# Optimization experiments

Hardware: AMD Instinct MI355X
Metric: run time of the kernel (lower is better)

## Reference

```python
import jax, jax.numpy as jnp
import numpy as np

B, N = 64, 196
D1, D2, H = 512, 2048, 512


def setup_inputs() -> dict:
    key = jax.random.key(0)
    ks = jax.random.split(key, 8)
    s1 = 1.0 / np.sqrt(D1)
    s2 = 1.0 / np.sqrt(D2)
    sh = 1.0 / np.sqrt(H)
    return {
        "input1": jax.random.normal(ks[0], (B, D1), jnp.float32),
        "input2": jax.random.normal(ks[1], (B, N, D2), jnp.float32),
        "W1": jax.random.uniform(ks[2], (D1, H), jnp.float32, -s1, s1),
        "b1": jax.random.uniform(ks[3], (H,), jnp.float32, -s1, s1),
        "W2": jax.random.uniform(ks[4], (D2, H), jnp.float32, -s2, s2),
        "b2": jax.random.uniform(ks[5], (H,), jnp.float32, -s2, s2),
        "Wf": jax.random.uniform(ks[6], (H, 1), jnp.float32, -sh, sh),
        "bf": jax.random.uniform(ks[7], (1,), jnp.float32, -sh, sh),
    }


def reference(input1, input2, W1, b1, W2, b2, Wf, bf):
    # enc1: [B, H]; enc2: [B, N, H]
    enc1 = input1 @ W1 + b1
    enc2 = jnp.einsum("bnd,dh->bnh", input2, W2) + b2
    # additive (Bahdanau) score: relu(enc2 + enc1[:,None]) @ Wf -> [B, N]
    scores = (jax.nn.relu(enc2 + enc1[:, None, :]) @ Wf)[..., 0] + bf[0]
    alpha = jax.nn.softmax(scores, axis=1)  # softmax over N regions
    att = jnp.einsum("bnd,bn->bd", input2, alpha)  # weighted sum of raw features
    return att, alpha
```

## Files before the change

### kernel.cpp

```cpp
#include <hip/hip_runtime.h>
#include <hip/hip_bf16.h>
#include <stdint.h>

#define BB 64
#define NN 196
#define D1c 512
#define D2c 2048
#define HHc 512
#define MM (BB*NN)

typedef __attribute__((ext_vector_type(8))) short bf16x8;
typedef __attribute__((ext_vector_type(4))) float f32x4;

__device__ inline ushort f2bf(float f){
  uint32_t u = __float_as_uint(f);
  u += 0x7fff + ((u >> 16) & 1);
  return (ushort)(u >> 16);
}
__device__ inline uint32_t pack2(float a, float b){
  return (uint32_t)f2bf(a) | ((uint32_t)f2bf(b) << 16);
}

__global__ __launch_bounds__(256) void w2t_kernel(const float* __restrict__ W2,
                                                  ushort* __restrict__ w2t){
  __shared__ float tile[64][65];
  const int kt = blockIdx.x;
  const int ht = blockIdx.y;
  const int t = threadIdx.x;
  const int tr = t >> 4;
  const int tc = (t & 15) * 4;
  #pragma unroll
  for (int p = 0; p < 4; ++p){
    int k = p*16 + tr;
    float4 v = *(const float4*)(W2 + (size_t)(kt*64 + k)*HHc + ht*64 + tc);
    tile[k][tc] = v.x; tile[k][tc+1] = v.y; tile[k][tc+2] = v.z; tile[k][tc+3] = v.w;
  }
  __syncthreads();
  #pragma unroll
  for (int p = 0; p < 4; ++p){
    int h = p*16 + tr;
    ushort4 o;
    o.x = f2bf(tile[tc  ][h]);
    o.y = f2bf(tile[tc+1][h]);
    o.z = f2bf(tile[tc+2][h]);
    o.w = f2bf(tile[tc+3][h]);
    *(ushort4*)(w2t + (size_t)(ht*64 + h)*D2c + kt*64 + tc) = o;
  }
}

__global__ __launch_bounds__(128) void enc1_kernel(const float* __restrict__ in1,
                                                   const float* __restrict__ W1,
                                                   const float* __restrict__ b1,
                                                   float* __restrict__ enc1){
  __shared__ float s1[D1c];
  const int b = blockIdx.x;
  const int ht = blockIdx.y;
  const int t = threadIdx.x;
  ((float4*)s1)[t] = ((const float4*)(in1 + (size_t)b*D1c))[t];
  __syncthreads();
  const int h = ht*128 + t;
  float acc = b1[h];
  #pragma unroll 8
  for (int d = 0; d < D1c; ++d)
    acc += s1[d] * W1[(size_t)d*HHc + h];
  enc1[b*HHc + h] = acc;
}

__global__ __launch_bounds__(256,2) void score_gemm(
    const float*  __restrict__ in2,
    const ushort* __restrict__ w2t,
    const float*  __restrict__ b2,
    const float*  __restrict__ wf,
    const float*  __restrict__ enc1,
    float*        __restrict__ scores)
{
  __shared__ ushort As[2][64*64];
  __shared__ ushort Bs[2][256*64];

  const int t = threadIdx.x;
  const int p  = blockIdx.x;
  const int lg = (p & 7) * 49 + (p >> 3);
  const int h0 = (lg & 1) * 256;
  const int m0 = (lg >> 1) * 64;

  const int wave = t >> 6, lane = t & 63;
  const int l15 = lane & 15, l4 = lane >> 4;

  const int arow = t >> 2;
  const int aq   = t & 3;
  const float* aBase = in2 + (size_t)(m0 + arow)*D2c + aq*16;
  const int ac0 = ((aq*2    ) ^ (arow & 7)) << 3;
  const int ac1 = ((aq*2 + 1) ^ (arow & 7)) << 3;

  const int bl_r = lane >> 3;
  const int bl_c = (lane & 7) ^ bl_r;

  float b2v[4], wfv[4];
  #pragma unroll
  for (int hf = 0; hf < 4; ++hf){
    int hc = h0 + wave*64 + hf*16 + l15;
    b2v[hf] = b2[hc]; wfv[hf] = wf[hc];
  }

  f32x4 acc[4][4];
  #pragma unroll
  for (int i = 0; i < 4; ++i)
    #pragma unroll
    for (int j = 0; j < 4; ++j) acc[i][j] = (f32x4)0.f;

  float4 aReg[4];

#define A_LOAD(kt)                                                           \
  { _Pragma("unroll")                                                        \
    for (int j = 0; j < 4; ++j)                                              \
      aReg[j] = *(const float4*)(aBase + (kt)*64 + j*4); }

#define A_WRITE(buf)                                                         \
  { uint4 w0, w1;                                                            \
    w0.x = pack2(aReg[0].x, aReg[0].y); w0.y = pack2(aReg[0].z, aReg[0].w);  \
    w0.z = pack2(aReg[1].x, aReg[1].y); w0.w = pack2(aReg[1].z, aReg[1].w);  \
    w1.x = pack2(aReg[2].x, aReg[2].y); w1.y = pack2(aReg[2].z, aReg[2].w);  \
    w1.z = pack2(aReg[3].x, aReg[3].y); w1.w = pack2(aReg[3].z, aReg[3].w);  \
    *(uint4*)(As[buf] + arow*64 + ac0) = w0;                                 \
    *(uint4*)(As[buf] + arow*64 + ac1) = w1; }

#define B_GLDS(kt, buf)                                                      \
  { _Pragma("unroll")                                                        \
    for (int i = 0; i < 8; ++i){                                             \
      const ushort* src = w2t + (size_t)(h0 + wave*64 + i*8 + bl_r)*D2c      \
                          + (kt)*64 + bl_c*8;                                \
      __builtin_amdgcn_global_load_lds(                                      \
          (const __attribute__((address_space(1))) uint32_t*)src,            \
          (__attribute__((address_space(3))) uint32_t*)(Bs[buf] + (wave*64 + i*8)*64), \
          16, 0, 0); } }

#define COMPUTE(buf)                                                         \
  { _Pragma("unroll")                                                        \
    for (int kk = 0; kk < 2; ++kk){                                          \
      bf16x8 af[4], bfr[4];                                                  \
      _Pragma("unroll")                                                      \
      for (int mf = 0; mf < 4; ++mf){                                        \
        int r = mf*16 + l15, c = kk*4 + l4;                                  \
        af[mf] = *(const bf16x8*)(As[buf] + r*64 + ((c ^ (r & 7)) << 3)); }  \
      _Pragma("unroll")                                                      \
      for (int hf = 0; hf < 4; ++hf){                                        \
        int r = wave*64 + hf*16 + l15, c = kk*4 + l4;                        \
        bfr[hf] = *(const bf16x8*)(Bs[buf] + r*64 + ((c ^ (r & 7)) << 3)); } \
      _Pragma("unroll")                                                      \
      for (int mf = 0; mf < 4; ++mf)                                         \
        _Pragma("unroll")                                                    \
        for (int hf = 0; hf < 4; ++hf)                                       \
          acc[mf][hf] = __builtin_amdgcn_mfma_f32_16x16x32_bf16(             \
              af[mf], bfr[hf], acc[mf][hf], 0, 0, 0); } }

#define SB0() __builtin_amdgcn_sched_barrier(0)
#define BAR() { SB0(); __builtin_amdgcn_s_barrier(); SB0(); }

  A_LOAD(0);
  SB0();
  B_GLDS(0, 0);
  asm volatile("s_waitcnt vmcnt(8)" ::: "memory");
  SB0();
  A_WRITE(0);
  asm volatile("s_waitcnt lgkmcnt(0)" ::: "memory");
  BAR();

  for (int kt = 0; kt < 31; ++kt){
    const int cur = kt & 1;
    A_LOAD(kt + 1);
    SB0();
    B_GLDS(kt + 1, cur ^ 1);
    asm volatile("s_waitcnt vmcnt(12)" ::: "memory");
    BAR();
    COMPUTE(cur);
    asm volatile("s_waitcnt vmcnt(8)" ::: "memory");
    SB0();
    A_WRITE(cur ^ 1);
    asm volatile("s_waitcnt lgkmcnt(0)" ::: "memory");
    BAR();
  }
  asm volatile("s_waitcnt vmcnt(0)" ::: "memory");
  BAR();
  COMPUTE(1);

  #pragma unroll
  for (int mf = 0; mf < 4; ++mf){
    #pragma unroll
    for (int r = 0; r < 4; ++r){
      int m = m0 + mf*16 + l4*4 + r;
      int b = m / NN;
      const float* e1 = enc1 + (size_t)b*HHc + h0 + wave*64 + l15;
      float s = 0.f;
      #pragma unroll
      for (int hf = 0; hf < 4; ++hf){
        float v = acc[mf][hf][r] + b2v[hf] + e1[hf*16];
        s += fmaxf(v, 0.f) * wfv[hf];
      }
      s += __shfl_xor(s, 1); s += __shfl_xor(s, 2);
      s += __shfl_xor(s, 4); s += __shfl_xor(s, 8);
      if (l15 == 0) atomicAdd(&scores[m], s);
    }
  }
#undef A_LOAD
#undef A_WRITE
#undef B_GLDS
#undef COMPUTE
#undef SB0
#undef BAR
}

__global__ __launch_bounds__(64) void softmax_kernel(const float* __restrict__ scores,
                                                     float* __restrict__ alpha){
  const int b = blockIdx.x, t = threadIdx.x;
  const float* s = scores + b*NN;
  float x[4]; float mx = -1e30f;
  #pragma unroll
  for (int i = 0; i < 4; ++i){
    int n = t + i*64;
    x[i] = (n < NN) ? s[n] : -1e30f;
    mx = fmaxf(mx, x[i]);
  }
  #pragma unroll
  for (int o = 1; o < 64; o <<= 1) mx = fmaxf(mx, __shfl_xor(mx, o));
  float sum = 0.f;
  #pragma unroll
  for (int i = 0; i < 4; ++i){
    int n = t + i*64;
    float e = (n < NN) ? __expf(x[i] - mx) : 0.f;
    x[i] = e; sum += e;
  }
  #pragma unroll
  for (int o = 1; o < 64; o <<= 1) sum += __shfl_xor(sum, o);
  float inv = 1.f / sum;
  #pragma unroll
  for (int i = 0; i < 4; ++i){
    int n = t + i*64;
    if (n < NN) alpha[b*NN + n] = x[i] * inv;
  }
}

__global__ __launch_bounds__(256) void att_kernel(const float* __restrict__ in2,
                                                  const float* __restrict__ alpha,
                                                  float* __restrict__ att){
  __shared__ float sal[NN];
  const int b = blockIdx.y;
  const int t = threadIdx.x;
  if (t < NN) sal[t] = alpha[b*NN + t];
  __syncthreads();
  const int d = blockIdx.x*256 + t;
  const float* src = in2 + (size_t)b*NN*D2c + d;
  float acc = 0.f;
  #pragma unroll 7
  for (int n = 0; n < NN; ++n)
    acc += src[(size_t)n*D2c] * sal[n];
  att[(size_t)b*D2c + d] = acc;
}

extern "C" void kernel_launch(void* const* d_in, const int* in_sizes, int n_in,
                              void* d_out, int out_size, void* d_ws, size_t ws_size,
                              hipStream_t stream){
  (void)in_sizes; (void)n_in; (void)out_size; (void)ws_size;
  const float* input1 = (const float*)d_in[0];
  const float* input2 = (const float*)d_in[1];
  const float* W1     = (const float*)d_in[2];
  const float* b1     = (const float*)d_in[3];
  const float* W2     = (const float*)d_in[4];
  const float* b2     = (const float*)d_in[5];
  const float* Wf     = (const float*)d_in[6];

  float* out   = (float*)d_out;
  float* att   = out;
  float* alpha = out + BB*D2c;

  char*   ws     = (char*)d_ws;
  ushort* w2t    = (ushort*)ws;
  float*  enc1   = (float*)(ws + 2*1024*1024);
  float*  scores = (float*)(ws + 2*1024*1024 + 131072);

  hipMemsetAsync(scores, 0, MM*sizeof(float), stream);
  w2t_kernel<<<dim3(32, 8), 256, 0, stream>>>(W2, w2t);
  enc1_kernel<<<dim3(BB, 4), 128, 0, stream>>>(input1, W1, b1, enc1);
  score_gemm<<<dim3(392), 256, 0, stream>>>(input2, w2t, b2, Wf, enc1, scores);
  softmax_kernel<<<dim3(BB), 64, 0, stream>>>(scores, alpha);
  att_kernel<<<dim3(8, BB), 256, 0, stream>>>(input2, alpha, att);
}
```

Measured before the change: 112.8 us.

## Pre-swizzle W2 into MFMA fragment layout and load B directly to registers

```diff
diff --git a/kernel.cpp b/kernel.cpp
--- a/kernel.cpp
+++ b/kernel.cpp
@@ -24,27 +24,30 @@
 __global__ __launch_bounds__(256) void w2t_kernel(const float* __restrict__ W2,
                                                   ushort* __restrict__ w2t){
   __shared__ float tile[64][65];
-  const int kt = blockIdx.x;
-  const int ht = blockIdx.y;
+  const int ktb = blockIdx.x;
+  const int ht  = blockIdx.y;
   const int t = threadIdx.x;
   const int tr = t >> 4;
   const int tc = (t & 15) * 4;
   #pragma unroll
   for (int p = 0; p < 4; ++p){
     int k = p*16 + tr;
-    float4 v = *(const float4*)(W2 + (size_t)(kt*64 + k)*HHc + ht*64 + tc);
+    float4 v = *(const float4*)(W2 + (size_t)(ktb*64 + k)*HHc + ht*64 + tc);
     tile[k][tc] = v.x; tile[k][tc+1] = v.y; tile[k][tc+2] = v.z; tile[k][tc+3] = v.w;
   }
   __syncthreads();
   #pragma unroll
-  for (int p = 0; p < 4; ++p){
-    int h = p*16 + tr;
+  for (int pp = 0; pp < 4; ++pp){
+    int hl = pp*16 + tr;
     ushort4 o;
-    o.x = f2bf(tile[tc  ][h]);
-    o.y = f2bf(tile[tc+1][h]);
-    o.z = f2bf(tile[tc+2][h]);
-    o.w = f2bf(tile[tc+3][h]);
-    *(ushort4*)(w2t + (size_t)(ht*64 + h)*D2c + kt*64 + tc) = o;
+    o.x = f2bf(tile[tc  ][hl]);
+    o.y = f2bf(tile[tc+1][hl]);
+    o.z = f2bf(tile[tc+2][hl]);
+    o.w = f2bf(tile[tc+3][hl]);
+    size_t addr = (size_t)(ht*4 + pp)*32768 + (size_t)ktb*1024
+                + (size_t)((tc>>5)&1)*512 + (size_t)((tc>>3)&3)*128
+                + (size_t)tr*8 + (tc & 4);
+    *(ushort4*)(w2t + addr) = o;
   }
 }
 
@@ -66,7 +69,7 @@
   enc1[b*HHc + h] = acc;
 }
 
-__global__ __launch_bounds__(256,2) void score_gemm(
+__global__ __launch_bounds__(256) void score_gemm(
     const float*  __restrict__ in2,
     const ushort* __restrict__ w2t,
     const float*  __restrict__ b2,
@@ -75,7 +78,6 @@
     float*        __restrict__ scores)
 {
   __shared__ ushort As[2][64*64];
-  __shared__ ushort Bs[2][256*64];
 
   const int t = threadIdx.x;
   const int p  = blockIdx.x;
@@ -92,8 +94,7 @@
   const int ac0 = ((aq*2    ) ^ (arow & 7)) << 3;
   const int ac1 = ((aq*2 + 1) ^ (arow & 7)) << 3;
 
-  const int bl_r = lane >> 3;
-  const int bl_c = (lane & 7) ^ bl_r;
+  const ushort* bBase = w2t + (size_t)h0*2048 + (size_t)wave*131072 + lane*8;
 
   float b2v[4], wfv[4];
   #pragma unroll
@@ -109,11 +110,17 @@
     for (int j = 0; j < 4; ++j) acc[i][j] = (f32x4)0.f;
 
   float4 aReg[4];
+  bf16x8 bA[8], bB[8];
 
 #define A_LOAD(kt)                                                           \
   { _Pragma("unroll")                                                        \
     for (int j = 0; j < 4; ++j)                                              \
       aReg[j] = *(const float4*)(aBase + (kt)*64 + j*4); }
+
+#define B_LOAD(kt, B)                                                        \
+  { _Pragma("unroll")                                                        \
+    for (int f = 0; f < 8; ++f)                                              \
+      B[f] = *(const bf16x8*)(bBase + (f>>1)*32768 + (kt)*1024 + (f&1)*512); }
 
 #define A_WRITE(buf)                                                         \
   { uint4 w0, w1;                                                            \
@@ -124,64 +131,53 @@
     *(uint4*)(As[buf] + arow*64 + ac0) = w0;                                 \
     *(uint4*)(As[buf] + arow*64 + ac1) = w1; }
 
-#define B_GLDS(kt, buf)                                                      \
-  { _Pragma("unroll")                                                        \
-    for (int i = 0; i < 8; ++i){                                             \
-      const ushort* src = w2t + (size_t)(h0 + wave*64 + i*8 + bl_r)*D2c      \
-                          + (kt)*64 + bl_c*8;                                \
-      __builtin_amdgcn_global_load_lds(                                      \
-          (const __attribute__((address_space(1))) uint32_t*)src,            \
-          (__attribute__((address_space(3))) uint32_t*)(Bs[buf] + (wave*64 + i*8)*64), \
-          16, 0, 0); } }
-
-#define COMPUTE(buf)                                                         \
+#define COMPUTE(buf, B)                                                      \
   { _Pragma("unroll")                                                        \
     for (int kk = 0; kk < 2; ++kk){                                          \
-      bf16x8 af[4], bfr[4];                                                  \
+      bf16x8 af[4];                                                          \
       _Pragma("unroll")                                                      \
       for (int mf = 0; mf < 4; ++mf){                                        \
         int r = mf*16 + l15, c = kk*4 + l4;                                  \
         af[mf] = *(const bf16x8*)(As[buf] + r*64 + ((c ^ (r & 7)) << 3)); }  \
       _Pragma("unroll")                                                      \
-      for (int hf = 0; hf < 4; ++hf){                                        \
-        int r = wave*64 + hf*16 + l15, c = kk*4 + l4;                        \
-        bfr[hf] = *(const bf16x8*)(Bs[buf] + r*64 + ((c ^ (r & 7)) << 3)); } \
-      _Pragma("unroll")                                                      \
       for (int mf = 0; mf < 4; ++mf)                                         \
         _Pragma("unroll")                                                    \
         for (int hf = 0; hf < 4; ++hf)                                       \
           acc[mf][hf] = __builtin_amdgcn_mfma_f32_16x16x32_bf16(             \
-              af[mf], bfr[hf], acc[mf][hf], 0, 0, 0); } }
-
-#define SB0() __builtin_amdgcn_sched_barrier(0)
-#define BAR() { SB0(); __builtin_amdgcn_s_barrier(); SB0(); }
+              af[mf], B[hf*2+kk], acc[mf][hf], 0, 0, 0); } }
+
+#define LGKM0() asm volatile("s_waitcnt lgkmcnt(0)" ::: "memory")
+#define SB0()   __builtin_amdgcn_sched_barrier(0)
+#define BAR()   { SB0(); __builtin_amdgcn_s_barrier(); SB0(); }
 
   A_LOAD(0);
-  SB0();
-  B_GLDS(0, 0);
-  asm volatile("s_waitcnt vmcnt(8)" ::: "memory");
-  SB0();
+  B_LOAD(0, bA);
   A_WRITE(0);
-  asm volatile("s_waitcnt lgkmcnt(0)" ::: "memory");
+  LGKM0();
   BAR();
 
-  for (int kt = 0; kt < 31; ++kt){
-    const int cur = kt & 1;
+  #pragma unroll 1
+  for (int kt = 0; kt < 30; kt += 2){
     A_LOAD(kt + 1);
-    SB0();
-    B_GLDS(kt + 1, cur ^ 1);
-    asm volatile("s_waitcnt vmcnt(12)" ::: "memory");
+    B_LOAD(kt + 1, bB);
+    COMPUTE(0, bA);
+    A_WRITE(1);
+    LGKM0();
     BAR();
-    COMPUTE(cur);
-    asm volatile("s_waitcnt vmcnt(8)" ::: "memory");
-    SB0();
-    A_WRITE(cur ^ 1);
-    asm volatile("s_waitcnt lgkmcnt(0)" ::: "memory");
+    A_LOAD(kt + 2);
+    B_LOAD(kt + 2, bA);
+    COMPUTE(1, bB);
+    A_WRITE(0);
+    LGKM0();
     BAR();
   }
-  asm volatile("s_waitcnt vmcnt(0)" ::: "memory");
+  A_LOAD(31);
+  B_LOAD(31, bB);
+  COMPUTE(0, bA);
+  A_WRITE(1);
+  LGKM0();
   BAR();
-  COMPUTE(1);
+  COMPUTE(1, bB);
 
   #pragma unroll
   for (int mf = 0; mf < 4; ++mf){
@@ -202,9 +198,10 @@
     }
   }
 #undef A_LOAD
+#undef B_LOAD
 #undef A_WRITE
-#undef B_GLDS
 #undef COMPUTE
+#undef LGKM0
 #undef SB0
 #undef BAR
 }
```

Result: faster. 105.3 us (-6.7%).

## Enlarge score GEMM tile to 128x256 with 8 waves and hardware bf16 pack

Applied to the files above, without the earlier changes.

```diff
diff --git a/kernel.cpp b/kernel.cpp
--- a/kernel.cpp
+++ b/kernel.cpp
@@ -17,8 +17,10 @@
   u += 0x7fff + ((u >> 16) & 1);
   return (ushort)(u >> 16);
 }
-__device__ inline uint32_t pack2(float a, float b){
-  return (uint32_t)f2bf(a) | ((uint32_t)f2bf(b) << 16);
+__device__ inline uint32_t cvtpk(float lo, float hi){
+  uint32_t r;
+  asm("v_cvt_pk_bf16_f32 %0, %1, %2" : "=v"(r) : "v"(lo), "v"(hi));
+  return r;
 }
 
 __global__ __launch_bounds__(256) void w2t_kernel(const float* __restrict__ W2,
@@ -66,7 +68,7 @@
   enc1[b*HHc + h] = acc;
 }
 
-__global__ __launch_bounds__(256,2) void score_gemm(
+__global__ __launch_bounds__(512,2) void score_gemm(
     const float*  __restrict__ in2,
     const ushort* __restrict__ w2t,
     const float*  __restrict__ b2,
@@ -74,23 +76,24 @@
     const float*  __restrict__ enc1,
     float*        __restrict__ scores)
 {
-  __shared__ ushort As[2][64*64];
+  __shared__ ushort As[2][128*64];
   __shared__ ushort Bs[2][256*64];
 
   const int t = threadIdx.x;
-  const int p  = blockIdx.x;
-  const int lg = (p & 7) * 49 + (p >> 3);
-  const int h0 = (lg & 1) * 256;
-  const int m0 = (lg >> 1) * 64;
+  const int p   = blockIdx.x;
+  const int xcd = p & 7;
+  const int lg  = (xcd < 4 ? xcd*25 : 100 + (xcd-4)*24) + (p >> 3);
+  const int h0  = (lg & 1) * 256;
+  const int m0  = (lg >> 1) * 128;
 
   const int wave = t >> 6, lane = t & 63;
+  const int wm = wave >> 2, whh = wave & 3;
   const int l15 = lane & 15, l4 = lane >> 4;
 
-  const int arow = t >> 2;
-  const int aq   = t & 3;
-  const float* aBase = in2 + (size_t)(m0 + arow)*D2c + aq*16;
-  const int ac0 = ((aq*2    ) ^ (arow & 7)) << 3;
-  const int ac1 = ((aq*2 + 1) ^ (arow & 7)) << 3;
+  const int rA = wave*16 + l4;
+  const float* aBase = in2 + (size_t)(m0 + rA)*D2c + l15*4;
+  const int acw  = l15 >> 1;
+  const int apar = (l15 & 1) * 4;
 
   const int bl_r = lane >> 3;
   const int bl_c = (lane & 7) ^ bl_r;
@@ -98,7 +101,7 @@
   float b2v[4], wfv[4];
   #pragma unroll
   for (int hf = 0; hf < 4; ++hf){
-    int hc = h0 + wave*64 + hf*16 + l15;
+    int hc = h0 + whh*64 + hf*16 + l15;
     b2v[hf] = b2[hc]; wfv[hf] = wf[hc];
   }
 
@@ -113,25 +116,26 @@
 #define A_LOAD(kt)                                                           \
   { _Pragma("unroll")                                                        \
     for (int j = 0; j < 4; ++j)                                              \
-      aReg[j] = *(const float4*)(aBase + (kt)*64 + j*4); }
+      aReg[j] = *(const float4*)(aBase + (size_t)(j*4)*D2c + (kt)*64); }
 
 #define A_WRITE(buf)                                                         \
-  { uint4 w0, w1;                                                            \
-    w0.x = pack2(aReg[0].x, aReg[0].y); w0.y = pack2(aReg[0].z, aReg[0].w);  \
-    w0.z = pack2(aReg[1].x, aReg[1].y); w0.w = pack2(aReg[1].z, aReg[1].w);  \
-    w1.x = pack2(aReg[2].x, aReg[2].y); w1.y = pack2(aReg[2].z, aReg[2].w);  \
-    w1.z = pack2(aReg[3].x, aReg[3].y); w1.w = pack2(aReg[3].z, aReg[3].w);  \
-    *(uint4*)(As[buf] + arow*64 + ac0) = w0;                                 \
-    *(uint4*)(As[buf] + arow*64 + ac1) = w1; }
+  { _Pragma("unroll")                                                        \
+    for (int j = 0; j < 4; ++j){                                             \
+      int r = rA + j*4;                                                      \
+      uint2 pk;                                                              \
+      pk.x = cvtpk(aReg[j].x, aReg[j].y);                                    \
+      pk.y = cvtpk(aReg[j].z, aReg[j].w);                                    \
+      *(uint2*)(As[buf] + r*64 + ((acw ^ (r & 7)) << 3) + apar) = pk; } }
 
 #define B_GLDS(kt, buf)                                                      \
   { _Pragma("unroll")                                                        \
-    for (int i = 0; i < 8; ++i){                                             \
-      const ushort* src = w2t + (size_t)(h0 + wave*64 + i*8 + bl_r)*D2c      \
+    for (int i = 0; i < 4; ++i){                                             \
+      int g = wave*4 + i;                                                    \
+      const ushort* src = w2t + (size_t)(h0 + g*8 + bl_r)*D2c                \
                           + (kt)*64 + bl_c*8;                                \
       __builtin_amdgcn_global_load_lds(                                      \
           (const __attribute__((address_space(1))) uint32_t*)src,            \
-          (__attribute__((address_space(3))) uint32_t*)(Bs[buf] + (wave*64 + i*8)*64), \
+          (__attribute__((address_space(3))) uint32_t*)(Bs[buf] + g*512),    \
           16, 0, 0); } }
 
 #define COMPUTE(buf)                                                         \
@@ -140,11 +144,11 @@
       bf16x8 af[4], bfr[4];                                                  \
       _Pragma("unroll")                                                      \
       for (int mf = 0; mf < 4; ++mf){                                        \
-        int r = mf*16 + l15, c = kk*4 + l4;                                  \
+        int r = wm*64 + mf*16 + l15, c = kk*4 + l4;                          \
         af[mf] = *(const bf16x8*)(As[buf] + r*64 + ((c ^ (r & 7)) << 3)); }  \
       _Pragma("unroll")                                                      \
       for (int hf = 0; hf < 4; ++hf){                                        \
-        int r = wave*64 + hf*16 + l15, c = kk*4 + l4;                        \
+        int r = whh*64 + hf*16 + l15, c = kk*4 + l4;                         \
         bfr[hf] = *(const bf16x8*)(Bs[buf] + r*64 + ((c ^ (r & 7)) << 3)); } \
       _Pragma("unroll")                                                      \
       for (int mf = 0; mf < 4; ++mf)                                         \
@@ -153,33 +157,31 @@
           acc[mf][hf] = __builtin_amdgcn_mfma_f32_16x16x32_bf16(             \
               af[mf], bfr[hf], acc[mf][hf], 0, 0, 0); } }
 
-#define SB0() __builtin_amdgcn_sched_barrier(0)
-#define BAR() { SB0(); __builtin_amdgcn_s_barrier(); SB0(); }
+#define SB0()    __builtin_amdgcn_sched_barrier(0)
+#define WAITV(n) { asm volatile("s_waitcnt vmcnt(" #n ")" ::: "memory"); SB0(); }
+#define LGKM0()  { asm volatile("s_waitcnt lgkmcnt(0)" ::: "memory"); SB0(); }
+#define BAR()    { SB0(); __builtin_amdgcn_s_barrier(); SB0(); }
 
   A_LOAD(0);
-  SB0();
   B_GLDS(0, 0);
-  asm volatile("s_waitcnt vmcnt(8)" ::: "memory");
-  SB0();
+  WAITV(4);
   A_WRITE(0);
-  asm volatile("s_waitcnt lgkmcnt(0)" ::: "memory");
+  LGKM0();
   BAR();
 
+  #pragma unroll 1
   for (int kt = 0; kt < 31; ++kt){
-    const int cur = kt & 1;
     A_LOAD(kt + 1);
-    SB0();
-    B_GLDS(kt + 1, cur ^ 1);
-    asm volatile("s_waitcnt vmcnt(12)" ::: "memory");
+    B_GLDS(kt + 1, (kt + 1) & 1);
+    WAITV(8);
     BAR();
-    COMPUTE(cur);
-    asm volatile("s_waitcnt vmcnt(8)" ::: "memory");
-    SB0();
-    A_WRITE(cur ^ 1);
-    asm volatile("s_waitcnt lgkmcnt(0)" ::: "memory");
+    COMPUTE(kt & 1);
+    WAITV(4);
+    A_WRITE((kt + 1) & 1);
+    LGKM0();
     BAR();
   }
-  asm volatile("s_waitcnt vmcnt(0)" ::: "memory");
+  WAITV(0);
   BAR();
   COMPUTE(1);
 
@@ -187,9 +189,9 @@
   for (int mf = 0; mf < 4; ++mf){
     #pragma unroll
     for (int r = 0; r < 4; ++r){
-      int m = m0 + mf*16 + l4*4 + r;
+      int m = m0 + wm*64 + mf*16 + l4*4 + r;
       int b = m / NN;
-      const float* e1 = enc1 + (size_t)b*HHc + h0 + wave*64 + l15;
+      const float* e1 = enc1 + (size_t)b*HHc + h0 + whh*64 + l15;
       float s = 0.f;
       #pragma unroll
       for (int hf = 0; hf < 4; ++hf){
@@ -205,6 +207,8 @@
 #undef A_WRITE
 #undef B_GLDS
 #undef COMPUTE
+#undef WAITV
+#undef LGKM0
 #undef SB0
 #undef BAR
 }
@@ -280,7 +284,7 @@
   hipMemsetAsync(scores, 0, MM*sizeof(float), stream);
   w2t_kernel<<<dim3(32, 8), 256, 0, stream>>>(W2, w2t);
   enc1_kernel<<<dim3(BB, 4), 128, 0, stream>>>(input1, W1, b1, enc1);
-  score_gemm<<<dim3(392), 256, 0, stream>>>(input2, w2t, b2, Wf, enc1, scores);
+  score_gemm<<<dim3(196), 512, 0, stream>>>(input2, w2t, b2, Wf, enc1, scores);
   softmax_kernel<<<dim3(BB), 64, 0, stream>>>(scores, alpha);
   att_kernel<<<dim3(8, BB), 256, 0, stream>>>(input2, alpha, att);
 }
```

Result: faster. 109.8 us (-2.7%).
